# Optimization experiments

Measured on AMD Instinct MI355X. Metric: run time of the kernel, lower is better.

Reference implementation:

```python
import jax, jax.numpy as jnp
import numpy as np

N = 32       # number of variables (per-var LSTMs)
L = 128      # window length
D = 128      # hidden dim
HEADS = 8
TAU_MAX = 5
ALPHA = 0.7  # attn_decay_alpha
B = 128      # number of time-ordered windows


def setup_inputs() -> dict:
    key = jax.random.key(0)
    ks = jax.random.split(key, 20)
    s = 0.1
    f = lambda k, shape: (jax.random.normal(k, shape, jnp.float32) * s)
    return {
        "X": jax.random.normal(ks[0], (B, L, N), jnp.float32),
        # per-variable encoder LSTM (input size 1): W_ih (N,4D), W_hh (N,4D,D), combined-style biases kept separate
        "enc_Wih": f(ks[1], (N, 4 * D)),
        "enc_Whh": f(ks[2], (N, 4 * D, D)),
        "enc_b": f(ks[3], (N, 4 * D)),            # b_ih + b_hh merged (mathematically identical)
        "pool_w": f(ks[4], (N, D)),
        "pool_b": f(ks[5], (N,)),
        # shared MultiheadAttention params (torch layout: in_proj (3D,D))
        "in_proj_w": f(ks[6], (3 * D, D)),
        "in_proj_b": f(ks[7], (3 * D,)),
        "out_proj_w": f(ks[8], (D, D)),
        "out_proj_b": f(ks[9], (D,)),
        # per-variable decoder: init_h/init_c Linear(d,d), LSTM(1,d) (input is all-zeros so W_ih drops out), out Linear(d,1)
        "dec_initH_w": f(ks[10], (N, D, D)),
        "dec_initH_b": f(ks[11], (N, D)),
        "dec_initC_w": f(ks[12], (N, D, D)),
        "dec_initC_b": f(ks[13], (N, D)),
        "dec_Whh": f(ks[14], (N, 4 * D, D)),
        "dec_bih": f(ks[15], (N, 4 * D)),
        "dec_bhh": f(ks[16], (N, 4 * D)),
        "dec_out_w": f(ks[17], (N, D)),
        "dec_out_b": f(ks[18], (N,)),
    }


def _lstm_cell(gates, c):
    # torch gate order: i, f, g, o
    i, fg, g, o = jnp.split(gates, 4, axis=-1)
    i = jax.nn.sigmoid(i); fg = jax.nn.sigmoid(fg)
    g = jnp.tanh(g); o = jax.nn.sigmoid(o)
    c = fg * c + i * g
    h = o * jnp.tanh(c)
    return h, c


def _encode(X, Wih, Whh, b, pool_w, pool_b):
    # X: (B,L,N); encoder consumes first L-1 steps of each variable, batched over all N vars
    x = jnp.transpose(X[:, :-1, :], (1, 2, 0))  # (T, N, B)
    Bn = X.shape[0]
    h0 = jnp.zeros((N, Bn, D), X.dtype)

    def step(carry, x_t):  # x_t: (N,B)
        h, c = carry
        gates = (x_t[..., None] * Wih[:, None, :]
                 + jnp.einsum('nbd,ngd->nbg', h, Whh)
                 + b[:, None, :])
        h, c = _lstm_cell(gates, c)
        return (h, c), h

    _, H = jax.lax.scan(step, (h0, h0), x)  # H: (T,N,B,D)
    # TemporalAttnPool: softmax over time of a linear score, weighted sum
    scores = jnp.einsum('tnbd,nd->tnb', H, pool_w) + pool_b[None, :, None]
    a = jax.nn.softmax(scores, axis=0)
    C = jnp.einsum('tnb,tnbd->bnd', a, H)  # (B,N,D)
    return C


def _mha(Q, KV, in_w, in_b, out_w, out_b):
    dh = D // HEADS
    q = Q @ in_w[:D].T + in_b[:D]
    k = KV @ in_w[D:2 * D].T + in_b[D:2 * D]
    v = KV @ in_w[2 * D:].T + in_b[2 * D:]
    sp = lambda x: x.reshape(x.shape[0], x.shape[1], HEADS, dh)
    q, k, v = sp(q), sp(k), sp(v)
    scores = jnp.einsum('bqhd,bkhd->bhqk', q, k) / float(np.sqrt(dh))
    attn = jax.nn.softmax(scores, axis=-1)
    o = jnp.einsum('bhqk,bkhd->bqhd', attn, v).reshape(Q.shape)
    return o @ out_w.T + out_b


def _cross_attend(C, in_w, in_b, out_w, out_b):
    Bn = C.shape[0]
    tmax = min(TAU_MAX, Bn - 1)
    if tmax <= 0:
        return C
    out_sum = jnp.zeros_like(C)
    w_sum = jnp.zeros((Bn, 1, 1), C.dtype)
    for tau in range(1, tmax + 1):  # small fixed loop over lags
        o = _mha(C[tau:], C[:-tau], in_w, in_b, out_w, out_b)
        w = float(np.exp(-ALPHA * (tau - 1)))  # attn_agg == 'decay'
        out_sum = out_sum.at[tau:].add(o * w)
        w_sum = w_sum.at[tau:].add(w)
    out = out_sum / jnp.clip(w_sum, 1e-8)
    return C + out  # residual=True


def _decode(C_star, iHw, iHb, iCw, iCb, Whh, bih, bhh, ow, ob):
    # h0/c0 from tanh(Linear(c_star)); LSTM input is all-zeros so input term reduces to b_ih
    h0 = jnp.tanh(jnp.einsum('bnd,ned->nbe', C_star, iHw) + iHb[:, None, :])
    c0 = jnp.tanh(jnp.einsum('bnd,ned->nbe', C_star, iCw) + iCb[:, None, :])
    b = (bih + bhh)[:, None, :]  # (N,1,4D)

    def step(carry, _):
        h, c = carry
        gates = jnp.einsum('nbd,ngd->nbg', h, Whh) + b
        h, c = _lstm_cell(gates, c)
        o = jnp.einsum('nbd,nd->nb', h, ow) + ob[:, None]
        return (h, c), o

    _, O = jax.lax.scan(step, (h0, c0), None, length=L)  # (L,N,B)
    recon = jnp.transpose(O[:L - 1], (2, 0, 1))  # (B,L-1,N)
    pred = O[L - 1].T                            # (B,N)
    return recon, pred


def reference(X, enc_Wih, enc_Whh, enc_b, pool_w, pool_b,
              in_proj_w, in_proj_b, out_proj_w, out_proj_b,
              dec_initH_w, dec_initH_b, dec_initC_w, dec_initC_b,
              dec_Whh, dec_bih, dec_bhh, dec_out_w, dec_out_b):
    C = _encode(X, enc_Wih, enc_Whh, enc_b, pool_w, pool_b)
    C_star = _cross_attend(C, in_proj_w, in_proj_b, out_proj_w, out_proj_b)
    recon, pred = _decode(C_star, dec_initH_w, dec_initH_b, dec_initC_w, dec_initC_b,
                          dec_Whh, dec_bih, dec_bhh, dec_out_w, dec_out_b)
    return recon, pred, C_star
```

## Files before the change

kernel.cpp:

```cpp
#include <hip/hip_runtime.h>
#include <hip/hip_bf16.h>

typedef unsigned short ushort_t;
typedef unsigned int uint_t;

#define DD   128
#define G4   512
#define BT   16
#define NB   128
#define NV   32

#define OFF_WIH   0
#define OFF_EB    16384
#define OFF_PW    32768
#define OFF_PB    36864
#define OFF_INW   36896
#define OFF_INB   86048
#define OFF_OUTW  86432
#define OFF_OUTB  102816
#define OFF_IHB   102944
#define OFF_ICB   107040
#define OFF_DBIH  111136
#define OFF_DBHH  127520
#define OFF_DOW   143904
#define OFF_DOB   148000
#define P_TOTAL   148032
#define X_TOTAL   (NB * 128 * NV)

typedef __attribute__((ext_vector_type(8))) short bf16x8;
typedef __attribute__((ext_vector_type(4))) float f32x4;

__device__ __forceinline__ float bf2f(ushort_t u) {
    union { uint_t i; float f; } x; x.i = ((uint_t)u) << 16; return x.f;
}
__device__ __forceinline__ float bflo(uint_t u) {
    union { uint_t i; float f; } x; x.i = u << 16; return x.f;
}
__device__ __forceinline__ float bfhi(uint_t u) {
    union { uint_t i; float f; } x; x.i = u & 0xffff0000u; return x.f;
}
__device__ __forceinline__ ushort_t f2bf(float f) {
    __hip_bfloat16 h = __float2bfloat16(f);
    return *(ushort_t*)&h;
}
__device__ __forceinline__ uint_t f2u(float f) {
    union { float f; uint_t i; } x; x.f = f; return x.i;
}
__device__ __forceinline__ float u2f(uint_t u) {
    union { uint_t i; float f; } x; x.i = u; return x.f;
}
__device__ __forceinline__ float sigmoid_f(float x) {
    return __builtin_amdgcn_rcpf(1.f + __expf(-x));
}
__device__ __forceinline__ float tanh_f(float x) {
    float e = __expf(2.f * x);
    return 1.f - 2.f * __builtin_amdgcn_rcpf(e + 1.f);
}
__device__ __forceinline__ float swz_bcast16(float v) {
    return u2f((uint_t)__builtin_amdgcn_ds_swizzle((int)f2u(v), 0x0010));
}
__device__ __forceinline__ void store_out(void* out, long idx, float v, int bf) {
    if (bf) ((ushort_t*)out)[idx] = f2bf(v);
    else    ((float*)out)[idx]    = v;
}

struct Ptr19 { const void* p[19]; int e[19]; };

__global__ __launch_bounds__(64) void probe_kernel(Ptr19 a, int* __restrict__ flags) {
    int i = blockIdx.x;
    int t = threadIdx.x;
    int cap = a.e[i] < 2048 ? a.e[i] : 2048;
    int cnt = 0, tot = 0;
    const ushort_t* p = (const ushort_t*)a.p[i];
    for (int j = t; j < cap; j += 64) {
        ushort_t u = p[j];
        float af = fabsf(bf2f(u));
        tot++;
        if (u == 0 || (af > 1e-7f && af < 100.f)) cnt++;
    }
    #pragma unroll
    for (int off = 32; off >= 1; off >>= 1) {
        cnt += __shfl_xor(cnt, off);
        tot += __shfl_xor(tot, off);
    }
    if (t == 0) flags[i] = (cnt * 10 >= tot * 9) ? 1 : 0;
}

__global__ __launch_bounds__(256) void conv_all(Ptr19 a, const int* __restrict__ flags,
                                                float* __restrict__ P, float* __restrict__ Xc) {
    int i = blockIdx.x * 256 + threadIdx.x;
    if (i < P_TOTAL) {
        int src, off;
        if      (i < OFF_EB)   { src = 1;  off = i - OFF_WIH; }
        else if (i < OFF_PW)   { src = 3;  off = i - OFF_EB; }
        else if (i < OFF_PB)   { src = 4;  off = i - OFF_PW; }
        else if (i < OFF_INW)  { src = 5;  off = i - OFF_PB; }
        else if (i < OFF_INB)  { src = 6;  off = i - OFF_INW; }
        else if (i < OFF_OUTW) { src = 7;  off = i - OFF_INB; }
        else if (i < OFF_OUTB) { src = 8;  off = i - OFF_OUTW; }
        else if (i < OFF_IHB)  { src = 9;  off = i - OFF_OUTB; }
        else if (i < OFF_ICB)  { src = 11; off = i - OFF_IHB; }
        else if (i < OFF_DBIH) { src = 13; off = i - OFF_ICB; }
        else if (i < OFF_DBHH) { src = 15; off = i - OFF_DBIH; }
        else if (i < OFF_DOW)  { src = 16; off = i - OFF_DBHH; }
        else if (i < OFF_DOB)  { src = 17; off = i - OFF_DOW; }
        else                   { src = 18; off = i - OFF_DOB; }
        int bf = flags[src];
        P[i] = bf ? bf2f(((const ushort_t*)a.p[src])[off]) : ((const float*)a.p[src])[off];
    } else if (i < P_TOTAL + X_TOTAL) {
        int j = i - P_TOTAL;
        int b = j & 127, nn = (j >> 7) & 31, t = j >> 12;
        int si = b * 4096 + t * 32 + nn;
        int bf = flags[0];
        Xc[j] = bf ? bf2f(((const ushort_t*)a.p[0])[si]) : ((const float*)a.p[0])[si];
    }
}

__global__ __launch_bounds__(512, 2) void enc_kernel(
    const float* __restrict__ Xc, const void* __restrict__ Wraw,
    const int* __restrict__ flags, const float* __restrict__ P,
    float* __restrict__ Cout)
{
    const int n = blockIdx.y, b0 = blockIdx.x * BT;
    const int tid = threadIdx.x;
    const int w = tid >> 6, lane = tid & 63;
    const int l15 = lane & 15, quad = lane >> 4;
    const int wbf = flags[2];
    const int d_own = 16 * w + l15;

    __shared__ alignas(16) ushort_t hS[2][16 * 136];

    for (int i = tid; i < 16 * 136; i += 512) hS[0][i] = 0;

    bf16x8 bfrag[4][4];
    #pragma unroll
    for (int typ = 0; typ < 4; typ++) {
        const int g = typ * 128 + d_own;
        #pragma unroll
        for (int kc = 0; kc < 4; kc++) {
            const int base = (n * G4 + g) * DD + 32 * kc + 8 * quad;
            if (wbf) {
                bfrag[typ][kc] = *(const bf16x8*)((const ushort_t*)Wraw + base);
            } else {
                const float* fp = (const float*)Wraw + base;
                bf16x8 tmp;
                #pragma unroll
                for (int j = 0; j < 8; j++) tmp[j] = (short)f2bf(fp[j]);
                bfrag[typ][kc] = tmp;
            }
        }
    }

    bf16x8 pfrag[4];
    #pragma unroll
    for (int kc = 0; kc < 4; kc++) {
        bf16x8 tmp;
        #pragma unroll
        for (int j = 0; j < 8; j++)
            tmp[j] = (l15 == 0) ? (short)f2bf(P[OFF_PW + n * DD + 32 * kc + 8 * quad + j]) : (short)0;
        pfrag[kc] = tmp;
    }

    float bias[4], wih[4];
    #pragma unroll
    for (int typ = 0; typ < 4; typ++) {
        bias[typ] = P[OFF_EB  + n * G4 + typ * 128 + d_own];
        wih[typ]  = P[OFF_WIH + n * G4 + typ * 128 + d_own];
    }
    const float pb_r = P[OFF_PB + n];

    float cst[4], hprev[4], Cacc[4], lR[4];
    #pragma unroll
    for (int r = 0; r < 4; r++) {
        cst[r] = 0.f; hprev[r] = 0.f; Cacc[r] = 0.f; lR[r] = 0.f;
    }

    float4 xq = *(const float4*)&Xc[n * 128 + b0 + 4 * quad];

    for (int t = 0; t < 127; t++) {
        const int rb = t & 1, wb = rb ^ 1;
        __syncthreads();

        bf16x8 ah[4];
        #pragma unroll
        for (int kc = 0; kc < 4; kc++)
            ah[kc] = *(const bf16x8*)&hS[rb][l15 * 136 + 32 * kc + 8 * quad];

        f32x4 acc[4], accP;
        #pragma unroll
        for (int typ = 0; typ < 4; typ++) {
            f32x4 a;
            a.x = bias[typ] + xq.x * wih[typ];
            a.y = bias[typ] + xq.y * wih[typ];
            a.z = bias[typ] + xq.z * wih[typ];
            a.w = bias[typ] + xq.w * wih[typ];
            acc[typ] = a;
        }
        accP.x = pb_r; accP.y = pb_r; accP.z = pb_r; accP.w = pb_r;

        if (t < 126)
            xq = *(const float4*)&Xc[(t + 1) * 4096 + n * 128 + b0 + 4 * quad];

        #pragma unroll
        for (int kc = 0; kc < 4; kc++) {
            #pragma unroll
            for (int typ = 0; typ < 4; typ++)
                acc[typ] = __builtin_amdgcn_mfma_f32_16x16x32_bf16(ah[kc], bfrag[typ][kc], acc[typ], 0, 0, 0);
            accP = __builtin_amdgcn_mfma_f32_16x16x32_bf16(ah[kc], pfrag[kc], accP, 0, 0, 0);
        }

        if (t > 0) {
            #pragma unroll
            for (int r = 0; r < 4; r++) {
                float e = __expf(swz_bcast16(accP[r]));
                lR[r] += e;
                Cacc[r] = fmaf(e, hprev[r], Cacc[r]);
            }
        }

        float hn[4];
        #pragma unroll
        for (int r = 0; r < 4; r++) {
            float ii = sigmoid_f(acc[0][r]);
            float ff = sigmoid_f(acc[1][r]);
            float g2 = tanh_f(acc[2][r]);
            float oo = sigmoid_f(acc[3][r]);
            float cc = ff * cst[r] + ii * g2;
            cst[r] = cc;
            hn[r] = oo * tanh_f(cc);
        }

        #pragma unroll
        for (int r = 0; r < 4; r++)
            hS[wb][(4 * quad + r) * 136 + d_own] = f2bf(hn[r]);

        #pragma unroll
        for (int r = 0; r < 4; r++) hprev[r] = hn[r];
    }

    __syncthreads();
    {
        f32x4 accP;
        accP.x = pb_r; accP.y = pb_r; accP.z = pb_r; accP.w = pb_r;
        #pragma unroll
        for (int kc = 0; kc < 4; kc++) {
            bf16x8 ah = *(const bf16x8*)&hS[1][l15 * 136 + 32 * kc + 8 * quad];
            accP = __builtin_amdgcn_mfma_f32_16x16x32_bf16(ah, pfrag[kc], accP, 0, 0, 0);
        }
        #pragma unroll
        for (int r = 0; r < 4; r++) {
            float e = __expf(swz_bcast16(accP[r]));
            lR[r] += e;
            Cacc[r] = fmaf(e, hprev[r], Cacc[r]);
        }
    }
    #pragma unroll
    for (int r = 0; r < 4; r++)
        Cout[(b0 + 4 * quad + r) * (NV * DD) + n * DD + d_own] = Cacc[r] / lR[r];
}

__global__ __launch_bounds__(256) void qkv_kernel(
    const float* __restrict__ C, const float* __restrict__ P,
    float* __restrict__ q, float* __restrict__ k, float* __restrict__ v)
{
    int b = blockIdx.x, p = blockIdx.y, tid = threadIdx.x;
    int j = tid & 127, half = tid >> 7;
    __shared__ float Cb[NV * DD];
    for (int i = tid; i < NV * DD; i += 256) Cb[i] = C[b * (NV * DD) + i];
    __syncthreads();

    const float* wrow = P + OFF_INW + (p * DD + j) * DD;
    float bias = P[OFF_INB + p * DD + j];
    float acc[16];
    #pragma unroll
    for (int nn = 0; nn < 16; nn++) acc[nn] = bias;

    for (int dc = 0; dc < DD; dc += 8) {
        float4 w0 = *(const float4*)&wrow[dc];
        float4 w1 = *(const float4*)&wrow[dc + 4];
        #pragma unroll
        for (int nn = 0; nn < 16; nn++) {
            const float* cb = &Cb[(half * 16 + nn) * DD + dc];
            float4 c0 = *(float4*)&cb[0];
            float4 c1 = *(float4*)&cb[4];
            acc[nn] += c0.x * w0.x + c0.y * w0.y + c0.z * w0.z + c0.w * w0.w
                     + c1.x * w1.x + c1.y * w1.y + c1.z * w1.z + c1.w * w1.w;
        }
    }
    float* dst = (p == 0) ? q : (p == 1) ? k : v;
    for (int nn = 0; nn < 16; nn++)
        dst[b * (NV * DD) + (half * 16 + nn) * DD + j] = acc[nn];
}

__global__ __launch_bounds__(256) void attn_kernel(
    const float* __restrict__ q, const float* __restrict__ k, const float* __restrict__ v,
    const float* __restrict__ C, const float* __restrict__ P,
    const int* __restrict__ flags, float* __restrict__ Cstar, void* __restrict__ dout)
{
    int b = blockIdx.x, tid = threadIdx.x;
    int obf = flags[0];
    __shared__ float Qs[NV * DD], Ks[NV * DD], Vs[NV * DD];
    float* Os = Ks;
    for (int i = tid; i < NV * DD; i += 256) Qs[i] = q[b * (NV * DD) + i];
    __syncthreads();

    int hh = tid >> 5, qi = tid & 31;
    float qreg[16];
    #pragma unroll
    for (int u = 0; u < 4; u++) {
        float4 t4 = *(float4*)&Qs[qi * DD + hh * 16 + 4 * u];
        qreg[4*u] = t4.x; qreg[4*u+1] = t4.y; qreg[4*u+2] = t4.z; qreg[4*u+3] = t4.w;
    }

    float Oacc[16];
    #pragma unroll
    for (int u = 0; u < 16; u++) Oacc[u] = 0.f;
    float wsum = 0.f;
    int tmax = (b < 5) ? b : 5;

    for (int tau = 1; tau <= tmax; tau++) {
        __syncthreads();
        for (int i = tid; i < NV * DD; i += 256) {
            Ks[i] = k[(b - tau) * (NV * DD) + i];
            Vs[i] = v[(b - tau) * (NV * DD) + i];
        }
        __syncthreads();

        float s[NV];
        #pragma unroll
        for (int kk = 0; kk < NV; kk++) {
            float a = 0.f;
            #pragma unroll
            for (int u = 0; u < 4; u++) {
                float4 kv = *(float4*)&Ks[kk * DD + hh * 16 + 4 * u];
                a += qreg[4*u] * kv.x + qreg[4*u+1] * kv.y
                   + qreg[4*u+2] * kv.z + qreg[4*u+3] * kv.w;
            }
            s[kk] = a * 0.25f;
        }
        float mm = s[0];
        #pragma unroll
        for (int kk = 1; kk < NV; kk++) mm = fmaxf(mm, s[kk]);
        float ssum = 0.f;
        #pragma unroll
        for (int kk = 0; kk < NV; kk++) { s[kk] = __expf(s[kk] - mm); ssum += s[kk]; }
        float wdk = __expf(-0.7f * (float)(tau - 1));
        wsum += wdk;
        float wr = wdk / ssum;
        #pragma unroll
        for (int u = 0; u < 4; u++) {
            float ax = 0.f, ay = 0.f, az = 0.f, aw = 0.f;
            #pragma unroll
            for (int kk = 0; kk < NV; kk++) {
                float4 vv = *(float4*)&Vs[kk * DD + hh * 16 + 4 * u];
                ax += s[kk] * vv.x; ay += s[kk] * vv.y;
                az += s[kk] * vv.z; aw += s[kk] * vv.w;
            }
            Oacc[4*u] += wr * ax; Oacc[4*u+1] += wr * ay;
            Oacc[4*u+2] += wr * az; Oacc[4*u+3] += wr * aw;
        }
    }

    __syncthreads();
    float winv = (b > 0) ? 1.f / wsum : 0.f;
    #pragma unroll
    for (int u = 0; u < 16; u++)
        Os[qi * DD + hh * 16 + u] = Oacc[u] * winv;
    __syncthreads();

    int j = tid & 127, ng = tid >> 7;
    const float* wrow = P + OFF_OUTW + j * DD;
    float obias = P[OFF_OUTB + j];
    for (int nn = ng * 16; nn < ng * 16 + 16; nn++) {
        float a = (b > 0) ? obias : 0.f;
        for (int dc = 0; dc < DD; dc += 8) {
            float4 w0 = *(const float4*)&wrow[dc];
            float4 w1 = *(const float4*)&wrow[dc + 4];
            float4 o0 = *(float4*)&Os[nn * DD + dc];
            float4 o1 = *(float4*)&Os[nn * DD + dc + 4];
            a += o0.x*w0.x + o0.y*w0.y + o0.z*w0.z + o0.w*w0.w
               + o1.x*w1.x + o1.y*w1.y + o1.z*w1.z + o1.w*w1.w;
        }
        float cs = C[b * (NV * DD) + nn * DD + j] + a;
        Cstar[b * (NV * DD) + nn * DD + j] = cs;
        store_out(dout, 524288 + b * (NV * DD) + nn * DD + j, cs, obf);
    }
}

__global__ __launch_bounds__(512, 2) void dec_kernel(
    const float* __restrict__ Cstar,
    const void* __restrict__ iHw, const void* __restrict__ iCw,
    const void* __restrict__ Wraw, const int* __restrict__ flags,
    const float* __restrict__ P, void* __restrict__ out)
{
    const int n = blockIdx.y, b0 = blockIdx.x * BT;
    const int tid = threadIdx.x;
    const int w = tid >> 6, lane = tid & 63;
    const int l15 = lane & 15, quad = lane >> 4;
    const int wbf = flags[14], obf = flags[0];
    const int d_own = 16 * w + l15;

    __shared__ alignas(16) ushort_t hS[2][16 * 136];

    bf16x8 af[4];
    #pragma unroll
    for (int kc = 0; kc < 4; kc++) {
        const float* cp = &Cstar[(b0 + l15) * (NV * DD) + n * DD + 32 * kc + 8 * quad];
        float4 c0v = *(const float4*)&cp[0];
        float4 c1v = *(const float4*)&cp[4];
        bf16x8 tmp;
        tmp[0] = (short)f2bf(c0v.x); tmp[1] = (short)f2bf(c0v.y);
        tmp[2] = (short)f2bf(c0v.z); tmp[3] = (short)f2bf(c0v.w);
        tmp[4] = (short)f2bf(c1v.x); tmp[5] = (short)f2bf(c1v.y);
        tmp[6] = (short)f2bf(c1v.z); tmp[7] = (short)f2bf(c1v.w);
        af[kc] = tmp;
    }
    float cst[4];
    {
        const int hbf = flags[10], cbf = flags[12];
        f32x4 hAcc, cAcc;
        float hb = P[OFF_IHB + n * DD + d_own];
        float cb = P[OFF_ICB + n * DD + d_own];
        hAcc.x = hb; hAcc.y = hb; hAcc.z = hb; hAcc.w = hb;
        cAcc.x = cb; cAcc.y = cb; cAcc.z = cb; cAcc.w = cb;
        #pragma unroll
        for (int kc = 0; kc < 4; kc++) {
            const int base = (n * DD + d_own) * DD + 32 * kc + 8 * quad;
            bf16x8 wB;
            if (hbf) wB = *(const bf16x8*)((const ushort_t*)iHw + base);
            else {
                const float* fp = (const float*)iHw + base;
                #pragma unroll
                for (int j = 0; j < 8; j++) wB[j] = (short)f2bf(fp[j]);
            }
            hAcc = __builtin_amdgcn_mfma_f32_16x16x32_bf16(af[kc], wB, hAcc, 0, 0, 0);
            if (cbf) wB = *(const bf16x8*)((const ushort_t*)iCw + base);
            else {
                const float* fp = (const float*)iCw + base;
                #pragma unroll
                for (int j = 0; j < 8; j++) wB[j] = (short)f2bf(fp[j]);
            }
            cAcc = __builtin_amdgcn_mfma_f32_16x16x32_bf16(af[kc], wB, cAcc, 0, 0, 0);
        }
        #pragma unroll
        for (int r = 0; r < 4; r++) {
            float hv = tanh_f(hAcc[r]);
            cst[r]   = tanh_f(cAcc[r]);
            hS[0][(4 * quad + r) * 136 + d_own] = f2bf(hv);
        }
    }

    bf16x8 bfrag[4][4];
    #pragma unroll
    for (int typ = 0; typ < 4; typ++) {
        const int g = typ * 128 + d_own;
        #pragma unroll
        for (int kc = 0; kc < 4; kc++) {
            const int base = (n * G4 + g) * DD + 32 * kc + 8 * quad;
            if (wbf) {
                bfrag[typ][kc] = *(const bf16x8*)((const ushort_t*)Wraw + base);
            } else {
                const float* fp = (const float*)Wraw + base;
                bf16x8 tmp;
                #pragma unroll
                for (int j = 0; j < 8; j++) tmp[j] = (short)f2bf(fp[j]);
                bfrag[typ][kc] = tmp;
            }
        }
    }

    bf16x8 pfrag[4];
    #pragma unroll
    for (int kc = 0; kc < 4; kc++) {
        bf16x8 tmp;
        #pragma unroll
        for (int j = 0; j < 8; j++)
            tmp[j] = (l15 == 0) ? (short)f2bf(P[OFF_DOW + n * DD + 32 * kc + 8 * quad + j]) : (short)0;
        pfrag[kc] = tmp;
    }

    float bias[4];
    #pragma unroll
    for (int typ = 0; typ < 4; typ++) {
        int g = n * G4 + typ * 128 + d_own;
        bias[typ] = P[OFF_DBIH + g] + P[OFF_DBHH + g];
    }
    const float ob_r = P[OFF_DOB + n];

    for (int t = 0; t < 128; t++) {
        const int rb = t & 1, wb = rb ^ 1;
        __syncthreads();

        bf16x8 ah[4];
        #pragma unroll
        for (int kc = 0; kc < 4; kc++)
            ah[kc] = *(const bf16x8*)&hS[rb][l15 * 136 + 32 * kc + 8 * quad];

        f32x4 acc[4];
        #pragma unroll
        for (int typ = 0; typ < 4; typ++) {
            f32x4 a;
            a.x = bias[typ]; a.y = bias[typ]; a.z = bias[typ]; a.w = bias[typ];
            acc[typ] = a;
        }

        #pragma unroll
        for (int kc = 0; kc < 4; kc++)
            #pragma unroll
            for (int typ = 0; typ < 4; typ++)
                acc[typ] = __builtin_amdgcn_mfma_f32_16x16x32_bf16(ah[kc], bfrag[typ][kc], acc[typ], 0, 0, 0);

        if (w == 0) {
            f32x4 accP;
            accP.x = ob_r; accP.y = ob_r; accP.z = ob_r; accP.w = ob_r;
            #pragma unroll
            for (int kc = 0; kc < 4; kc++)
                accP = __builtin_amdgcn_mfma_f32_16x16x32_bf16(ah[kc], pfrag[kc], accP, 0, 0, 0);
            if (t > 0 && l15 == 0) {
                #pragma unroll
                for (int r = 0; r < 4; r++) {
                    long b = b0 + 4 * quad + r;
                    store_out(out, b * 4064 + (long)(t - 1) * NV + n, accP[r], obf);
                }
            }
        }

        float hn[4];
        #pragma unroll
        for (int r = 0; r < 4; r++) {
            float ii = sigmoid_f(acc[0][r]);
            float ff = sigmoid_f(acc[1][r]);
            float g2 = tanh_f(acc[2][r]);
            float oo = sigmoid_f(acc[3][r]);
            float cc = ff * cst[r] + ii * g2;
            cst[r] = cc;
            hn[r] = oo * tanh_f(cc);
        }

        #pragma unroll
        for (int r = 0; r < 4; r++)
            hS[wb][(4 * quad + r) * 136 + d_own] = f2bf(hn[r]);
    }

    __syncthreads();
    if (w == 0) {
        f32x4 accP;
        accP.x = ob_r; accP.y = ob_r; accP.z = ob_r; accP.w = ob_r;
        #pragma unroll
        for (int kc = 0; kc < 4; kc++) {
            bf16x8 ah = *(const bf16x8*)&hS[0][l15 * 136 + 32 * kc + 8 * quad];
            accP = __builtin_amdgcn_mfma_f32_16x16x32_bf16(ah, pfrag[kc], accP, 0, 0, 0);
        }
        if (l15 == 0) {
            #pragma unroll
            for (int r = 0; r < 4; r++) {
                long b = b0 + 4 * quad + r;
                store_out(out, 520192 + b * NV + n, accP[r], obf);
            }
        }
    }
}

extern "C" void kernel_launch(void* const* d_in, const int* in_sizes, int n_in,
                              void* d_out, int out_size, void* d_ws, size_t ws_size,
                              hipStream_t stream) {
    char* ws = (char*)d_ws;
    float*    P    = (float*)(ws + 0);
    float*    Xc   = (float*)(ws + (1u << 20));
    float*    C    = (float*)(ws + (3u << 20));
    float*    qb   = (float*)(ws + (5u << 20));
    float*    kb   = (float*)(ws + (7u << 20));
    float*    vb   = (float*)(ws + (9u << 20));
    float*    Cst  = (float*)(ws + (11u << 20));
    int*      flags = (int*)(ws + (13u << 20));

    Ptr19 a;
    for (int i = 0; i < 19; i++) { a.p[i] = d_in[i]; a.e[i] = in_sizes[i]; }
    probe_kernel<<<19, 64, 0, stream>>>(a, flags);
    conv_all<<<(P_TOTAL + X_TOTAL + 255) / 256, 256, 0, stream>>>(a, flags, P, Xc);

    enc_kernel<<<dim3(8, 32), 512, 0, stream>>>(Xc, d_in[2], flags, P, C);
    qkv_kernel<<<dim3(128, 3), 256, 0, stream>>>(C, P, qb, kb, vb);
    attn_kernel<<<dim3(128), 256, 0, stream>>>(qb, kb, vb, C, P, flags, Cst, d_out);
    dec_kernel<<<dim3(8, 32), 512, 0, stream>>>(Cst, d_in[10], d_in[12], d_in[14], flags, P, d_out);
}
```

Measured before the change: 441.9 us.

## Swap MFMA operand roles in LSTM kernels and tile-transpose X input

The encoder and decoder LSTM recurrences swap MFMA operands so weights become the A operand and hidden state the B operand. Each lane then owns 4 consecutive hidden units for one batch element, which allows vectorized ushort4 shared-memory writes of h, f32x4 bias loads and f32x4 C stores. The per-step attention weight becomes a single swizzle broadcast per lane instead of four. The time loop is unrolled by two with constant buffer indices, and the X transpose moves into a separate shared-memory tiled kernel so global accesses coalesce. This adds one extra kernel launch and changes the shared-memory access pattern, which could introduce bank conflicts.

```diff
diff --git a/kernel.cpp b/kernel.cpp
--- a/kernel.cpp
+++ b/kernel.cpp
@@ -25,19 +25,12 @@
 #define OFF_DOW   143904
 #define OFF_DOB   148000
 #define P_TOTAL   148032
-#define X_TOTAL   (NB * 128 * NV)
 
 typedef __attribute__((ext_vector_type(8))) short bf16x8;
 typedef __attribute__((ext_vector_type(4))) float f32x4;
 
 __device__ __forceinline__ float bf2f(ushort_t u) {
     union { uint_t i; float f; } x; x.i = ((uint_t)u) << 16; return x.f;
-}
-__device__ __forceinline__ float bflo(uint_t u) {
-    union { uint_t i; float f; } x; x.i = u << 16; return x.f;
-}
-__device__ __forceinline__ float bfhi(uint_t u) {
-    union { uint_t i; float f; } x; x.i = u & 0xffff0000u; return x.f;
 }
 __device__ __forceinline__ ushort_t f2bf(float f) {
     __hip_bfloat16 h = __float2bfloat16(f);
@@ -56,8 +49,8 @@
     float e = __expf(2.f * x);
     return 1.f - 2.f * __builtin_amdgcn_rcpf(e + 1.f);
 }
-__device__ __forceinline__ float swz_bcast16(float v) {
-    return u2f((uint_t)__builtin_amdgcn_ds_swizzle((int)f2u(v), 0x0010));
+__device__ __forceinline__ float swz_bcast_l15(float v) {
+    return u2f((uint_t)__builtin_amdgcn_ds_swizzle((int)f2u(v), 0x000F));
 }
 __device__ __forceinline__ void store_out(void* out, long idx, float v, int bf) {
     if (bf) ((ushort_t*)out)[idx] = f2bf(v);
@@ -87,32 +80,49 @@
 }
 
 __global__ __launch_bounds__(256) void conv_all(Ptr19 a, const int* __restrict__ flags,
-                                                float* __restrict__ P, float* __restrict__ Xc) {
+                                                float* __restrict__ P) {
     int i = blockIdx.x * 256 + threadIdx.x;
-    if (i < P_TOTAL) {
-        int src, off;
-        if      (i < OFF_EB)   { src = 1;  off = i - OFF_WIH; }
-        else if (i < OFF_PW)   { src = 3;  off = i - OFF_EB; }
-        else if (i < OFF_PB)   { src = 4;  off = i - OFF_PW; }
-        else if (i < OFF_INW)  { src = 5;  off = i - OFF_PB; }
-        else if (i < OFF_INB)  { src = 6;  off = i - OFF_INW; }
-        else if (i < OFF_OUTW) { src = 7;  off = i - OFF_INB; }
-        else if (i < OFF_OUTB) { src = 8;  off = i - OFF_OUTW; }
-        else if (i < OFF_IHB)  { src = 9;  off = i - OFF_OUTB; }
-        else if (i < OFF_ICB)  { src = 11; off = i - OFF_IHB; }
-        else if (i < OFF_DBIH) { src = 13; off = i - OFF_ICB; }
-        else if (i < OFF_DBHH) { src = 15; off = i - OFF_DBIH; }
-        else if (i < OFF_DOW)  { src = 16; off = i - OFF_DBHH; }
-        else if (i < OFF_DOB)  { src = 17; off = i - OFF_DOW; }
-        else                   { src = 18; off = i - OFF_DOB; }
-        int bf = flags[src];
-        P[i] = bf ? bf2f(((const ushort_t*)a.p[src])[off]) : ((const float*)a.p[src])[off];
-    } else if (i < P_TOTAL + X_TOTAL) {
-        int j = i - P_TOTAL;
-        int b = j & 127, nn = (j >> 7) & 31, t = j >> 12;
-        int si = b * 4096 + t * 32 + nn;
-        int bf = flags[0];
-        Xc[j] = bf ? bf2f(((const ushort_t*)a.p[0])[si]) : ((const float*)a.p[0])[si];
+    if (i >= P_TOTAL) return;
+    int src, off;
+    if      (i < OFF_EB)   { src = 1;  off = i - OFF_WIH; }
+    else if (i < OFF_PW)   { src = 3;  off = i - OFF_EB; }
+    else if (i < OFF_PB)   { src = 4;  off = i - OFF_PW; }
+    else if (i < OFF_INW)  { src = 5;  off = i - OFF_PB; }
+    else if (i < OFF_INB)  { src = 6;  off = i - OFF_INW; }
+    else if (i < OFF_OUTW) { src = 7;  off = i - OFF_INB; }
+    else if (i < OFF_OUTB) { src = 8;  off = i - OFF_OUTW; }
+    else if (i < OFF_IHB)  { src = 9;  off = i - OFF_OUTB; }
+    else if (i < OFF_ICB)  { src = 11; off = i - OFF_IHB; }
+    else if (i < OFF_DBIH) { src = 13; off = i - OFF_ICB; }
+    else if (i < OFF_DBHH) { src = 15; off = i - OFF_DBIH; }
+    else if (i < OFF_DOW)  { src = 16; off = i - OFF_DBHH; }
+    else if (i < OFF_DOB)  { src = 17; off = i - OFF_DOW; }
+    else                   { src = 18; off = i - OFF_DOB; }
+    int bf = flags[src];
+    P[i] = bf ? bf2f(((const ushort_t*)a.p[src])[off]) : ((const float*)a.p[src])[off];
+}
+
+__global__ __launch_bounds__(256) void transpose_X(const void* __restrict__ src,
+                                                   const int* __restrict__ flags,
+                                                   float* __restrict__ Xc) {
+    __shared__ float tile[32][65];
+    int bt  = blockIdx.x * 32;
+    int tn0 = blockIdx.y * 64;
+    int bf = flags[0];
+    int tx = threadIdx.x & 63, ty = threadIdx.x >> 6;
+    #pragma unroll
+    for (int k = 0; k < 8; k++) {
+        int row = ty * 8 + k;
+        int idx = (bt + row) * 4096 + tn0 + tx;
+        tile[row][tx] = bf ? bf2f(((const ushort_t*)src)[idx]) : ((const float*)src)[idx];
+    }
+    __syncthreads();
+    int bx = threadIdx.x & 31, tyy = threadIdx.x >> 5;
+    #pragma unroll
+    for (int k = 0; k < 8; k++) {
+        int tn = tn0 + tyy * 8 + k;
+        int t = tn >> 5, nn = tn & 31;
+        Xc[t * 4096 + nn * 128 + bt + bx] = tile[bx][tyy * 8 + k];
     }
 }
 
@@ -126,27 +136,26 @@
     const int w = tid >> 6, lane = tid & 63;
     const int l15 = lane & 15, quad = lane >> 4;
     const int wbf = flags[2];
-    const int d_own = 16 * w + l15;
+    const int bown = b0 + l15;
 
     __shared__ alignas(16) ushort_t hS[2][16 * 136];
-
     for (int i = tid; i < 16 * 136; i += 512) hS[0][i] = 0;
 
-    bf16x8 bfrag[4][4];
+    bf16x8 afrag[4][4];
     #pragma unroll
     for (int typ = 0; typ < 4; typ++) {
-        const int g = typ * 128 + d_own;
+        const int g = typ * 128 + 16 * w + l15;
         #pragma unroll
         for (int kc = 0; kc < 4; kc++) {
             const int base = (n * G4 + g) * DD + 32 * kc + 8 * quad;
             if (wbf) {
-                bfrag[typ][kc] = *(const bf16x8*)((const ushort_t*)Wraw + base);
+                afrag[typ][kc] = *(const bf16x8*)((const ushort_t*)Wraw + base);
             } else {
                 const float* fp = (const float*)Wraw + base;
                 bf16x8 tmp;
                 #pragma unroll
                 for (int j = 0; j < 8; j++) tmp[j] = (short)f2bf(fp[j]);
-                bfrag[typ][kc] = tmp;
+                afrag[typ][kc] = tmp;
             }
         }
     }
@@ -157,86 +166,80 @@
         bf16x8 tmp;
         #pragma unroll
         for (int j = 0; j < 8; j++)
-            tmp[j] = (l15 == 0) ? (short)f2bf(P[OFF_PW + n * DD + 32 * kc + 8 * quad + j]) : (short)0;
+            tmp[j] = (l15 == 0 || l15 == 8)
+                   ? (short)f2bf(P[OFF_PW + n * DD + 32 * kc + 8 * quad + j]) : (short)0;
         pfrag[kc] = tmp;
     }
 
-    float bias[4], wih[4];
+    f32x4 bias4[4], wih4[4];
     #pragma unroll
     for (int typ = 0; typ < 4; typ++) {
-        bias[typ] = P[OFF_EB  + n * G4 + typ * 128 + d_own];
-        wih[typ]  = P[OFF_WIH + n * G4 + typ * 128 + d_own];
+        int base = n * G4 + typ * 128 + 16 * w + 4 * quad;
+        bias4[typ] = *(const f32x4*)&P[OFF_EB + base];
+        wih4[typ]  = *(const f32x4*)&P[OFF_WIH + base];
     }
     const float pb_r = P[OFF_PB + n];
 
-    float cst[4], hprev[4], Cacc[4], lR[4];
-    #pragma unroll
-    for (int r = 0; r < 4; r++) {
-        cst[r] = 0.f; hprev[r] = 0.f; Cacc[r] = 0.f; lR[r] = 0.f;
-    }
-
-    float4 xq = *(const float4*)&Xc[n * 128 + b0 + 4 * quad];
-
-    for (int t = 0; t < 127; t++) {
-        const int rb = t & 1, wb = rb ^ 1;
-        __syncthreads();
-
-        bf16x8 ah[4];
-        #pragma unroll
-        for (int kc = 0; kc < 4; kc++)
-            ah[kc] = *(const bf16x8*)&hS[rb][l15 * 136 + 32 * kc + 8 * quad];
-
-        f32x4 acc[4], accP;
-        #pragma unroll
-        for (int typ = 0; typ < 4; typ++) {
-            f32x4 a;
-            a.x = bias[typ] + xq.x * wih[typ];
-            a.y = bias[typ] + xq.y * wih[typ];
-            a.z = bias[typ] + xq.z * wih[typ];
-            a.w = bias[typ] + xq.w * wih[typ];
-            acc[typ] = a;
-        }
-        accP.x = pb_r; accP.y = pb_r; accP.z = pb_r; accP.w = pb_r;
-
-        if (t < 126)
-            xq = *(const float4*)&Xc[(t + 1) * 4096 + n * 128 + b0 + 4 * quad];
-
-        #pragma unroll
-        for (int kc = 0; kc < 4; kc++) {
-            #pragma unroll
-            for (int typ = 0; typ < 4; typ++)
-                acc[typ] = __builtin_amdgcn_mfma_f32_16x16x32_bf16(ah[kc], bfrag[typ][kc], acc[typ], 0, 0, 0);
-            accP = __builtin_amdgcn_mfma_f32_16x16x32_bf16(ah[kc], pfrag[kc], accP, 0, 0, 0);
-        }
-
-        if (t > 0) {
-            #pragma unroll
-            for (int r = 0; r < 4; r++) {
-                float e = __expf(swz_bcast16(accP[r]));
-                lR[r] += e;
-                Cacc[r] = fmaf(e, hprev[r], Cacc[r]);
-            }
-        }
-
-        float hn[4];
-        #pragma unroll
-        for (int r = 0; r < 4; r++) {
-            float ii = sigmoid_f(acc[0][r]);
-            float ff = sigmoid_f(acc[1][r]);
-            float g2 = tanh_f(acc[2][r]);
-            float oo = sigmoid_f(acc[3][r]);
-            float cc = ff * cst[r] + ii * g2;
-            cst[r] = cc;
-            hn[r] = oo * tanh_f(cc);
-        }
-
-        #pragma unroll
-        for (int r = 0; r < 4; r++)
-            hS[wb][(4 * quad + r) * 136 + d_own] = f2bf(hn[r]);
-
-        #pragma unroll
-        for (int r = 0; r < 4; r++) hprev[r] = hn[r];
-    }
+    float cst[4], hprev[4], Cacc[4], lR = 0.f;
+    #pragma unroll
+    for (int r = 0; r < 4; r++) { cst[r] = 0.f; hprev[r] = 0.f; Cacc[r] = 0.f; }
+
+    float xq = Xc[n * 128 + bown];
+
+#define ENC_STEP(T, RB)                                                              \
+    do {                                                                             \
+        __syncthreads();                                                             \
+        bf16x8 bh[4];                                                                \
+        _Pragma("unroll")                                                            \
+        for (int kc = 0; kc < 4; kc++)                                               \
+            bh[kc] = *(const bf16x8*)&hS[RB][l15 * 136 + 32 * kc + 8 * quad];        \
+        f32x4 acc[4], accP;                                                          \
+        _Pragma("unroll")                                                            \
+        for (int typ = 0; typ < 4; typ++) {                                          \
+            f32x4 a;                                                                 \
+            a.x = bias4[typ].x + xq * wih4[typ].x;                                   \
+            a.y = bias4[typ].y + xq * wih4[typ].y;                                   \
+            a.z = bias4[typ].z + xq * wih4[typ].z;                                   \
+            a.w = bias4[typ].w + xq * wih4[typ].w;                                   \
+            acc[typ] = a;                                                            \
+        }                                                                            \
+        accP.x = pb_r; accP.y = pb_r; accP.z = pb_r; accP.w = pb_r;                  \
+        if ((T) < 126) xq = Xc[((T) + 1) * 4096 + n * 128 + bown];                   \
+        _Pragma("unroll")                                                            \
+        for (int kc = 0; kc < 4; kc++) {                                             \
+            accP = __builtin_amdgcn_mfma_f32_16x16x32_bf16(pfrag[kc], bh[kc], accP, 0, 0, 0); \
+            _Pragma("unroll")                                                        \
+            for (int typ = 0; typ < 4; typ++)                                        \
+                acc[typ] = __builtin_amdgcn_mfma_f32_16x16x32_bf16(afrag[typ][kc], bh[kc], acc[typ], 0, 0, 0); \
+        }                                                                            \
+        if ((T) > 0) {                                                               \
+            float e = __expf(swz_bcast_l15(accP[0]));                                \
+            lR += e;                                                                 \
+            _Pragma("unroll")                                                        \
+            for (int r = 0; r < 4; r++) Cacc[r] = fmaf(e, hprev[r], Cacc[r]);        \
+        }                                                                            \
+        ushort4 hw;                                                                  \
+        _Pragma("unroll")                                                            \
+        for (int r = 0; r < 4; r++) {                                                \
+            float ii = sigmoid_f(acc[0][r]);                                         \
+            float ff = sigmoid_f(acc[1][r]);                                         \
+            float g2 = tanh_f(acc[2][r]);                                            \
+            float oo = sigmoid_f(acc[3][r]);                                         \
+            float cc = ff * cst[r] + ii * g2;                                        \
+            cst[r] = cc;                                                             \
+            float hh = oo * tanh_f(cc);                                              \
+            hprev[r] = hh;                                                           \
+            ((ushort_t*)&hw)[r] = f2bf(hh);                                          \
+        }                                                                            \
+        *(ushort4*)&hS[(RB) ^ 1][l15 * 136 + 16 * w + 4 * quad] = hw;                \
+    } while (0)
+
+    for (int tp = 0; tp < 63; tp++) {
+        ENC_STEP(2 * tp, 0);
+        ENC_STEP(2 * tp + 1, 1);
+    }
+    ENC_STEP(126, 0);
+#undef ENC_STEP
 
     __syncthreads();
     {
@@ -244,19 +247,18 @@
         accP.x = pb_r; accP.y = pb_r; accP.z = pb_r; accP.w = pb_r;
         #pragma unroll
         for (int kc = 0; kc < 4; kc++) {
-            bf16x8 ah = *(const bf16x8*)&hS[1][l15 * 136 + 32 * kc + 8 * quad];
-            accP = __builtin_amdgcn_mfma_f32_16x16x32_bf16(ah, pfrag[kc], accP, 0, 0, 0);
-        }
-        #pragma unroll
-        for (int r = 0; r < 4; r++) {
-            float e = __expf(swz_bcast16(accP[r]));
-            lR[r] += e;
-            Cacc[r] = fmaf(e, hprev[r], Cacc[r]);
-        }
-    }
-    #pragma unroll
-    for (int r = 0; r < 4; r++)
-        Cout[(b0 + 4 * quad + r) * (NV * DD) + n * DD + d_own] = Cacc[r] / lR[r];
+            bf16x8 bh = *(const bf16x8*)&hS[1][l15 * 136 + 32 * kc + 8 * quad];
+            accP = __builtin_amdgcn_mfma_f32_16x16x32_bf16(pfrag[kc], bh, accP, 0, 0, 0);
+        }
+        float e = __expf(swz_bcast_l15(accP[0]));
+        lR += e;
+        #pragma unroll
+        for (int r = 0; r < 4; r++) Cacc[r] = fmaf(e, hprev[r], Cacc[r]);
+    }
+    float inv = 1.f / lR;
+    f32x4 cv;
+    cv.x = Cacc[0] * inv; cv.y = Cacc[1] * inv; cv.z = Cacc[2] * inv; cv.w = Cacc[3] * inv;
+    *(f32x4*)&Cout[bown * (NV * DD) + n * DD + 16 * w + 4 * quad] = cv;
 }
 
 __global__ __launch_bounds__(256) void qkv_kernel(
@@ -398,73 +400,71 @@
     const int w = tid >> 6, lane = tid & 63;
     const int l15 = lane & 15, quad = lane >> 4;
     const int wbf = flags[14], obf = flags[0];
-    const int d_own = 16 * w + l15;
+    const int bown = b0 + l15;
 
     __shared__ alignas(16) ushort_t hS[2][16 * 136];
 
-    bf16x8 af[4];
+    bf16x8 cstB[4];
     #pragma unroll
     for (int kc = 0; kc < 4; kc++) {
-        const float* cp = &Cstar[(b0 + l15) * (NV * DD) + n * DD + 32 * kc + 8 * quad];
-        float4 c0v = *(const float4*)&cp[0];
-        float4 c1v = *(const float4*)&cp[4];
+        const float* cp = &Cstar[bown * (NV * DD) + n * DD + 32 * kc + 8 * quad];
+        f32x4 c0v = *(const f32x4*)&cp[0];
+        f32x4 c1v = *(const f32x4*)&cp[4];
         bf16x8 tmp;
         tmp[0] = (short)f2bf(c0v.x); tmp[1] = (short)f2bf(c0v.y);
         tmp[2] = (short)f2bf(c0v.z); tmp[3] = (short)f2bf(c0v.w);
         tmp[4] = (short)f2bf(c1v.x); tmp[5] = (short)f2bf(c1v.y);
         tmp[6] = (short)f2bf(c1v.z); tmp[7] = (short)f2bf(c1v.w);
-        af[kc] = tmp;
+        cstB[kc] = tmp;
     }
     float cst[4];
     {
         const int hbf = flags[10], cbf = flags[12];
-        f32x4 hAcc, cAcc;
-        float hb = P[OFF_IHB + n * DD + d_own];
-        float cb = P[OFF_ICB + n * DD + d_own];
-        hAcc.x = hb; hAcc.y = hb; hAcc.z = hb; hAcc.w = hb;
-        cAcc.x = cb; cAcc.y = cb; cAcc.z = cb; cAcc.w = cb;
+        f32x4 hAcc = *(const f32x4*)&P[OFF_IHB + n * DD + 16 * w + 4 * quad];
+        f32x4 cAcc = *(const f32x4*)&P[OFF_ICB + n * DD + 16 * w + 4 * quad];
         #pragma unroll
         for (int kc = 0; kc < 4; kc++) {
-            const int base = (n * DD + d_own) * DD + 32 * kc + 8 * quad;
-            bf16x8 wB;
-            if (hbf) wB = *(const bf16x8*)((const ushort_t*)iHw + base);
+            const int base = (n * DD + 16 * w + l15) * DD + 32 * kc + 8 * quad;
+            bf16x8 wA;
+            if (hbf) wA = *(const bf16x8*)((const ushort_t*)iHw + base);
             else {
                 const float* fp = (const float*)iHw + base;
                 #pragma unroll
-                for (int j = 0; j < 8; j++) wB[j] = (short)f2bf(fp[j]);
+                for (int j = 0; j < 8; j++) wA[j] = (short)f2bf(fp[j]);
             }
-            hAcc = __builtin_amdgcn_mfma_f32_16x16x32_bf16(af[kc], wB, hAcc, 0, 0, 0);
-            if (cbf) wB = *(const bf16x8*)((const ushort_t*)iCw + base);
+            hAcc = __builtin_amdgcn_mfma_f32_16x16x32_bf16(wA, cstB[kc], hAcc, 0, 0, 0);
+            if (cbf) wA = *(const bf16x8*)((const ushort_t*)iCw + base);
             else {
                 const float* fp = (const float*)iCw + base;
                 #pragma unroll
-                for (int j = 0; j < 8; j++) wB[j] = (short)f2bf(fp[j]);
+                for (int j = 0; j < 8; j++) wA[j] = (short)f2bf(fp[j]);
             }
-            cAcc = __builtin_amdgcn_mfma_f32_16x16x32_bf16(af[kc], wB, cAcc, 0, 0, 0);
-        }
+            cAcc = __builtin_amdgcn_mfma_f32_16x16x32_bf16(wA, cstB[kc], cAcc, 0, 0, 0);
+        }
+        ushort4 hw;
         #pragma unroll
         for (int r = 0; r < 4; r++) {
-            float hv = tanh_f(hAcc[r]);
-            cst[r]   = tanh_f(cAcc[r]);
-            hS[0][(4 * quad + r) * 136 + d_own] = f2bf(hv);
-        }
-    }
-
-    bf16x8 bfrag[4][4];
+            ((ushort_t*)&hw)[r] = f2bf(tanh_f(hAcc[r]));
+            cst[r] = tanh_f(cAcc[r]);
+        }
+        *(ushort4*)&hS[0][l15 * 136 + 16 * w + 4 * quad] = hw;
+    }
+
+    bf16x8 afrag[4][4];
     #pragma unroll
     for (int typ = 0; typ < 4; typ++) {
-        const int g = typ * 128 + d_own;
+        const int g = typ * 128 + 16 * w + l15;
         #pragma unroll
         for (int kc = 0; kc < 4; kc++) {
             const int base = (n * G4 + g) * DD + 32 * kc + 8 * quad;
             if (wbf) {
-                bfrag[typ][kc] = *(const bf16x8*)((const ushort_t*)Wraw + base);
+                afrag[typ][kc] = *(const bf16x8*)((const ushort_t*)Wraw + base);
             } else {
                 const float* fp = (const float*)Wraw + base;
                 bf16x8 tmp;
                 #pragma unroll
                 for (int j = 0; j < 8; j++) tmp[j] = (short)f2bf(fp[j]);
-                bfrag[typ][kc] = tmp;
+                afrag[typ][kc] = tmp;
             }
         }
     }
@@ -479,68 +479,60 @@
         pfrag[kc] = tmp;
     }
 
-    float bias[4];
+    f32x4 bias4[4];
     #pragma unroll
     for (int typ = 0; typ < 4; typ++) {
-        int g = n * G4 + typ * 128 + d_own;
-        bias[typ] = P[OFF_DBIH + g] + P[OFF_DBHH + g];
+        int base = n * G4 + typ * 128 + 16 * w + 4 * quad;
+        f32x4 b1 = *(const f32x4*)&P[OFF_DBIH + base];
+        f32x4 b2 = *(const f32x4*)&P[OFF_DBHH + base];
+        bias4[typ].x = b1.x + b2.x; bias4[typ].y = b1.y + b2.y;
+        bias4[typ].z = b1.z + b2.z; bias4[typ].w = b1.w + b2.w;
     }
     const float ob_r = P[OFF_DOB + n];
 
-    for (int t = 0; t < 128; t++) {
-        const int rb = t & 1, wb = rb ^ 1;
-        __syncthreads();
-
-        bf16x8 ah[4];
-        #pragma unroll
-        for (int kc = 0; kc < 4; kc++)
-            ah[kc] = *(const bf16x8*)&hS[rb][l15 * 136 + 32 * kc + 8 * quad];
-
-        f32x4 acc[4];
-        #pragma unroll
-        for (int typ = 0; typ < 4; typ++) {
-            f32x4 a;
-            a.x = bias[typ]; a.y = bias[typ]; a.z = bias[typ]; a.w = bias[typ];
-            acc[typ] = a;
-        }
-
-        #pragma unroll
-        for (int kc = 0; kc < 4; kc++)
-            #pragma unroll
-            for (int typ = 0; typ < 4; typ++)
-                acc[typ] = __builtin_amdgcn_mfma_f32_16x16x32_bf16(ah[kc], bfrag[typ][kc], acc[typ], 0, 0, 0);
-
-        if (w == 0) {
-            f32x4 accP;
-            accP.x = ob_r; accP.y = ob_r; accP.z = ob_r; accP.w = ob_r;
-            #pragma unroll
-            for (int kc = 0; kc < 4; kc++)
-                accP = __builtin_amdgcn_mfma_f32_16x16x32_bf16(ah[kc], pfrag[kc], accP, 0, 0, 0);
-            if (t > 0 && l15 == 0) {
-                #pragma unroll
-                for (int r = 0; r < 4; r++) {
-                    long b = b0 + 4 * quad + r;
-                    store_out(out, b * 4064 + (long)(t - 1) * NV + n, accP[r], obf);
-                }
-            }
-        }
-
-        float hn[4];
-        #pragma unroll
-        for (int r = 0; r < 4; r++) {
-            float ii = sigmoid_f(acc[0][r]);
-            float ff = sigmoid_f(acc[1][r]);
-            float g2 = tanh_f(acc[2][r]);
-            float oo = sigmoid_f(acc[3][r]);
-            float cc = ff * cst[r] + ii * g2;
-            cst[r] = cc;
-            hn[r] = oo * tanh_f(cc);
-        }
-
-        #pragma unroll
-        for (int r = 0; r < 4; r++)
-            hS[wb][(4 * quad + r) * 136 + d_own] = f2bf(hn[r]);
-    }
+#define DEC_STEP(T, RB)                                                              \
+    do {                                                                             \
+        __syncthreads();                                                             \
+        bf16x8 bh[4];                                                                \
+        _Pragma("unroll")                                                            \
+        for (int kc = 0; kc < 4; kc++)                                               \
+            bh[kc] = *(const bf16x8*)&hS[RB][l15 * 136 + 32 * kc + 8 * quad];        \
+        f32x4 acc[4];                                                                \
+        _Pragma("unroll")                                                            \
+        for (int typ = 0; typ < 4; typ++) acc[typ] = bias4[typ];                     \
+        _Pragma("unroll")                                                            \
+        for (int kc = 0; kc < 4; kc++)                                               \
+            _Pragma("unroll")                                                        \
+            for (int typ = 0; typ < 4; typ++)                                        \
+                acc[typ] = __builtin_amdgcn_mfma_f32_16x16x32_bf16(afrag[typ][kc], bh[kc], acc[typ], 0, 0, 0); \
+        if (w == 0) {                                                                \
+            f32x4 accP;                                                              \
+            accP.x = ob_r; accP.y = ob_r; accP.z = ob_r; accP.w = ob_r;              \
+            _Pragma("unroll")                                                        \
+            for (int kc = 0; kc < 4; kc++)                                           \
+                accP = __builtin_amdgcn_mfma_f32_16x16x32_bf16(pfrag[kc], bh[kc], accP, 0, 0, 0); \
+            if ((T) > 0 && quad == 0)                                                \
+                store_out(out, (long)bown * 4064 + (long)((T) - 1) * NV + n, accP[0], obf); \
+        }                                                                            \
+        ushort4 hw;                                                                  \
+        _Pragma("unroll")                                                            \
+        for (int r = 0; r < 4; r++) {                                                \
+            float ii = sigmoid_f(acc[0][r]);                                         \
+            float ff = sigmoid_f(acc[1][r]);                                         \
+            float g2 = tanh_f(acc[2][r]);                                            \
+            float oo = sigmoid_f(acc[3][r]);                                         \
+            float cc = ff * cst[r] + ii * g2;                                        \
+            cst[r] = cc;                                                             \
+            ((ushort_t*)&hw)[r] = f2bf(oo * tanh_f(cc));                             \
+        }                                                                            \
+        *(ushort4*)&hS[(RB) ^ 1][l15 * 136 + 16 * w + 4 * quad] = hw;                \
+    } while (0)
+
+    for (int tp = 0; tp < 64; tp++) {
+        DEC_STEP(2 * tp, 0);
+        DEC_STEP(2 * tp + 1, 1);
+    }
+#undef DEC_STEP
 
     __syncthreads();
     if (w == 0) {
@@ -548,16 +540,11 @@
         accP.x = ob_r; accP.y = ob_r; accP.z = ob_r; accP.w = ob_r;
         #pragma unroll
         for (int kc = 0; kc < 4; kc++) {
-            bf16x8 ah = *(const bf16x8*)&hS[0][l15 * 136 + 32 * kc + 8 * quad];
-            accP = __builtin_amdgcn_mfma_f32_16x16x32_bf16(ah, pfrag[kc], accP, 0, 0, 0);
-        }
-        if (l15 == 0) {
-            #pragma unroll
-            for (int r = 0; r < 4; r++) {
-                long b = b0 + 4 * quad + r;
-                store_out(out, 520192 + b * NV + n, accP[r], obf);
-            }
-        }
+            bf16x8 bh = *(const bf16x8*)&hS[0][l15 * 136 + 32 * kc + 8 * quad];
+            accP = __builtin_amdgcn_mfma_f32_16x16x32_bf16(pfrag[kc], bh, accP, 0, 0, 0);
+        }
+        if (quad == 0)
+            store_out(out, 520192 + (long)bown * NV + n, accP[0], obf);
     }
 }
 
@@ -577,7 +564,8 @@
     Ptr19 a;
     for (int i = 0; i < 19; i++) { a.p[i] = d_in[i]; a.e[i] = in_sizes[i]; }
     probe_kernel<<<19, 64, 0, stream>>>(a, flags);
-    conv_all<<<(P_TOTAL + X_TOTAL + 255) / 256, 256, 0, stream>>>(a, flags, P, Xc);
+    conv_all<<<(P_TOTAL + 255) / 256, 256, 0, stream>>>(a, flags, P);
+    transpose_X<<<dim3(4, 64), 256, 0, stream>>>(d_in[0], flags, Xc);
 
     enc_kernel<<<dim3(8, 32), 512, 0, stream>>>(Xc, d_in[2], flags, P, C);
     qkv_kernel<<<dim3(128, 3), 256, 0, stream>>>(C, P, qb, kb, vb);
```

Result: no change. 435.3 us (-1.5%).
